# Optimization experiments

Measured on AMD Instinct MI355X. Metric: run time of the kernel, lower is better.

## Reference

```python
import jax, jax.numpy as jnp
from jax import lax
import numpy as np

TAU_R = 1.0
TAU_W = 5.0
W_MIN, W_MAX = 0.0, 0.05
N_MBON, N_FBN, N_DAN, N_KC = 20, 60, 20, 200
N_RECUR = N_MBON + N_FBN + N_DAN
B, T = 256, 61


def setup_inputs() -> dict:
    key = jax.random.key(0)
    ks = jax.random.split(key, 8)
    r_kc = jax.random.uniform(ks[0], (B, N_KC, T), dtype=jnp.float32)
    r_ext = jax.random.uniform(ks[1], (B, 2, T), dtype=jnp.float32)
    time = jnp.arange(T, dtype=jnp.float32) * 0.5  # dt = 0.5
    # KC->MBON plastic weights start at the max value (0.05), as in init
    W0_W = jax.random.uniform(ks[2], (B, N_MBON, N_KC), dtype=jnp.float32) * W_MAX
    W0_w = jax.random.uniform(ks[3], (B, N_MBON, N_KC), dtype=jnp.float32) * W_MAX
    sqrt2 = np.sqrt(2.0)
    W_mbon = jax.random.normal(ks[4], (N_RECUR, N_MBON)) * np.sqrt(1.0 / (sqrt2 * N_MBON))
    W_fbn = jax.random.normal(ks[5], (N_RECUR, N_FBN)) * np.sqrt(1.0 / (sqrt2 * N_FBN))
    W_dan = jax.random.normal(ks[6], (N_RECUR, N_DAN)) * np.sqrt(1.0 / (sqrt2 * N_DAN))
    W_recur = jnp.concatenate([W_mbon, W_fbn, W_dan], axis=1).astype(jnp.float32)
    W_ext = jax.random.normal(ks[7], (N_FBN, 2), dtype=jnp.float32)
    bias = jnp.full((N_RECUR,), 0.1, dtype=jnp.float32)
    W_readout = jax.random.normal(jax.random.fold_in(key, 99), (1, N_MBON), dtype=jnp.float32) / np.sqrt(N_MBON)
    return {"r_kc": r_kc, "r_ext": r_ext, "time": time, "n_batch": B,
            "W0_W": W0_W, "W0_w": W0_w, "W_recur": W_recur, "W_ext": W_ext,
            "bias": bias, "W_readout": W_readout}


def reference(r_kc, r_ext, time, n_batch, W0_W, W0_w, W_recur, W_ext, bias, W_readout):
    n_mbon, n_kc = W0_W.shape[1], W0_W.shape[2]
    n_fbn = W_ext.shape[0]
    n_recur = W_recur.shape[0]
    n_dan = n_recur - n_mbon - n_fbn
    nb = r_kc.shape[0]
    dt = time[1] - time[0]

    # initial state: FBN/DAN at 0.1, MBON at 0
    r_init = jnp.full((nb, n_recur), 0.1, dtype=r_kc.dtype).at[:, :n_mbon].set(0.0)
    # DAN->MBON weights are zeroed
    Wr = W_recur.at[:n_mbon, -n_dan:].set(0.0)
    rbk0 = r_kc[:, :, 0]            # KC eligibility trace
    rbd0 = r_init[:, -n_dan:]       # DAN eligibility trace
    readout0 = jnp.einsum('om,bm->bo', W_readout, r_init[:, :n_mbon]).squeeze(-1)
    zeros_dan = jnp.zeros((nb, n_dan), dtype=r_kc.dtype)

    def step(carry, xs):
        r, W, wt, rbk, rbd = carry
        rk_t, re_t = xs                                   # [B,n_kc], [B,n_ext]
        I_kc = jnp.einsum('bmk,bk->bm', W, rk_t)          # KC -> MBON via plastic W
        I_fbn = jnp.einsum('fe,be->bf', W_ext, re_t)      # context -> FBN
        I_tot = jnp.concatenate([I_kc, I_fbn, zeros_dan], axis=1)
        Wr_prod = jnp.einsum('sr,br->bs', Wr, r)
        dr = (-r + jax.nn.relu(Wr_prod + bias + I_tot)) / TAU_R
        r_new = r + dr * dt
        # plasticity update (uses the *new* DAN activity)
        rbk_new = rbk + (rk_t - rbk) * dt / TAU_W
        r_dan = r_new[:, -n_dan:]
        rbd_new = rbd + (r_dan - rbd) * dt / TAU_W
        dw = (jnp.einsum('bd,bk->bdk', rbd_new, rk_t)
              - jnp.einsum('bd,bk->bdk', r_dan, rbk_new))
        wt_new = wt + dw * dt
        W_new = jnp.clip(W + (-W + wt_new) / TAU_W * dt, W_MIN, W_MAX)
        ro = jnp.einsum('om,bm->bo', W_readout, r_new[:, :n_mbon]).squeeze(-1)
        return (r_new, W_new, wt_new, rbk_new, rbd_new), (r_new, W_new, wt_new, ro)

    xs = (jnp.moveaxis(r_kc, 2, 0)[:-1], jnp.moveaxis(r_ext, 2, 0)[:-1])
    carry0 = (r_init, W0_W, W0_w, rbk0, rbd0)
    _, (r_s, W_s, wt_s, ro_s) = lax.scan(step, carry0, xs)
    r_series = jnp.concatenate([r_init[None], r_s], axis=0)    # [T,B,n_recur]
    W_series = jnp.concatenate([W0_W[None], W_s], axis=0)      # [T,B,n_mbon,n_kc]
    wt_series = jnp.concatenate([W0_w[None], wt_s], axis=0)    # [T,B,n_mbon,n_kc]
    readout = jnp.concatenate([readout0[None], ro_s], axis=0)  # [T,B]
    return r_series, W_series, wt_series, readout
```

## Files before the change

kernel.cpp:

```cpp
#include <hip/hip_runtime.h>


#define NKC   200
#define NREC  100
#define TSTEP 61
#define NSTEP 60
#define PSTR  52
#define NTHR  512

typedef float vfloat4 __attribute__((ext_vector_type(4)));

__device__ __forceinline__ void bar_lds() {
    __builtin_amdgcn_sched_barrier(0);
    asm volatile("s_waitcnt lgkmcnt(0)");
    __builtin_amdgcn_s_barrier();
    __builtin_amdgcn_sched_barrier(0);
}

__device__ __forceinline__ void nt_store4(float* p, float4 v) {
    vfloat4 t;
    t.x = v.x; t.y = v.y; t.z = v.z; t.w = v.w;
    __builtin_nontemporal_store(t, (vfloat4*)p);
}
__device__ __forceinline__ void nt_store1(float* p, float v) {
    __builtin_nontemporal_store(v, p);
}

__global__ __launch_bounds__(NTHR, 1) void cond_rnn_kernel(
    const float* __restrict__ r_kc, const float* __restrict__ r_ext,
    const float* __restrict__ timev, const float* __restrict__ W0_W,
    const float* __restrict__ W0_w, const float* __restrict__ W_recur,
    const float* __restrict__ W_ext, const float* __restrict__ bias,
    const float* __restrict__ W_readout, float* __restrict__ out, int B)
{
    int b = blockIdx.x;
    if ((B & 7) == 0) {
        const int cpx = B >> 3;
        b = (blockIdx.x & 7) * cpx + (blockIdx.x >> 3);
    }
    const int tid = threadIdx.x;
    const float dt  = timev[1] - timev[0];
    const float dtw = dt / 5.0f;

    __shared__ __align__(16) float s_rk[TSTEP * NKC];
    __shared__ __align__(16) float s_re[128];
    __shared__ __align__(16) float s_Wro[32];
    __shared__ __align__(16) float s_r[2][112];
    __shared__ __align__(16) float s_rbd[32];
    __shared__ __align__(16) float s_part[20 * PSTR];

    const float* rk_b = r_kc + (size_t)b * (NKC * TSTEP);
    for (int f = tid; f < NKC * TSTEP; f += NTHR) {
        int k = f / TSTEP, t = f - k * TSTEP;
        s_rk[t * NKC + k] = rk_b[f];
    }
    const float* re_b = r_ext + (size_t)b * (2 * TSTEP);
    if (tid < 2 * TSTEP) s_re[tid] = re_b[tid];

    float4 wrreg[25];
    if (tid < 100) {
        const float* wrow = W_recur + tid * NREC;
        #pragma unroll
        for (int j4 = 0; j4 < 25; ++j4)
            wrreg[j4] = *(const float4*)(wrow + 4 * j4);
        if (tid < 20) {
            #pragma unroll
            for (int j4 = 20; j4 < 25; ++j4) {
                wrreg[j4].x = 0.f; wrreg[j4].y = 0.f;
                wrreg[j4].z = 0.f; wrreg[j4].w = 0.f;
            }
        }
    }

    if (tid < 20)  s_Wro[tid] = W_readout[tid];
    if (tid < 100) s_r[0][tid] = (tid < 20) ? 0.f : 0.1f;
    if (tid < 20)  s_rbd[tid] = 0.1f;

    float my_bias = 0.f, we0 = 0.f, we1 = 0.f;
    if (tid < 100) my_bias = bias[tid];
    if (tid >= 20 && tid < 80) { we0 = W_ext[(tid - 20) * 2]; we1 = W_ext[(tid - 20) * 2 + 1]; }
    float rbd_mine = 0.1f;
    float r_mine   = (tid < 20) ? 0.f : 0.1f;

    float* out_r  = out;
    float* out_W  = out + (size_t)TSTEP * B * 100;
    float* out_wt = out_W + (size_t)TSTEP * B * 4000;
    float* out_ro = out_wt + (size_t)TSTEP * B * 4000;

    float4 Wreg[2], wtreg[2], rbkreg[2], rkc[2];
    const float* W0Wb = W0_W + (size_t)b * 4000;
    const float* W0wb = W0_w + (size_t)b * 4000;
    #pragma unroll
    for (int i = 0; i < 2; ++i) {
        int c = tid + NTHR * i;
        if (c < 1000) {
            Wreg[i]  = *(const float4*)(W0Wb + 4 * c);
            wtreg[i] = *(const float4*)(W0wb + 4 * c);
            nt_store4(out_W  + (size_t)b * 4000 + 4 * c, Wreg[i]);
            nt_store4(out_wt + (size_t)b * 4000 + 4 * c, wtreg[i]);
        }
    }
    if (tid < 100) nt_store1(out_r + (size_t)b * 100 + tid, r_mine);

    __syncthreads();

    #pragma unroll
    for (int i = 0; i < 2; ++i) {
        int c = tid + NTHR * i;
        if (c < 1000) {
            int k0 = (4 * c) % NKC;
            int m  = c / 50;
            float4 rk0 = *(const float4*)(s_rk + k0);
            rbkreg[i] = rk0;
            rkc[i]    = rk0;
            float4 w = Wreg[i];
            s_part[m * PSTR + (c % 50)] =
                w.x * rk0.x + w.y * rk0.y + w.z * rk0.z + w.w * rk0.w;
        }
    }
    if (tid == 255) {
        float ro = 0.f;
        #pragma unroll
        for (int mm = 0; mm < 20; ++mm) ro += s_Wro[mm] * s_r[0][mm];
        nt_store1(out_ro + b, ro);
    }
    __syncthreads();

    for (int it = 0; it < NSTEP; ++it) {
        const int cur = it & 1, nxt = cur ^ 1;

        if (tid < 100) {
            float acc = my_bias;
            if (tid < 20) {
                const float* pp = s_part + tid * PSTR;
                float4 s01 = *(const float4*)(pp + 0)  + *(const float4*)(pp + 4);
                float4 s23 = *(const float4*)(pp + 8)  + *(const float4*)(pp + 12);
                float4 s45 = *(const float4*)(pp + 16) + *(const float4*)(pp + 20);
                float4 s67 = *(const float4*)(pp + 24) + *(const float4*)(pp + 28);
                float4 s89 = *(const float4*)(pp + 32) + *(const float4*)(pp + 36);
                float4 sab = *(const float4*)(pp + 40) + *(const float4*)(pp + 44);
                float4 t0 = s01 + s23;
                float4 t1 = s45 + s67;
                float4 t2 = s89 + sab;
                float4 u  = t0 + t1;
                u = u + t2;
                float tail = (pp[48] + pp[49]);
                acc += ((u.x + u.y) + (u.z + u.w)) + tail;
            } else if (tid < 80) {
                acc = fmaf(we0, s_re[it], acc);
                acc = fmaf(we1, s_re[TSTEP + it], acc);
            }
            float a0 = 0.f, a1 = 0.f, a2 = 0.f, a3 = 0.f;
            #pragma unroll
            for (int j4 = 0; j4 < 24; j4 += 4) {
                {
                    float4 w4 = wrreg[j4];
                    float4 r4 = *(const float4*)(&s_r[cur][4 * j4]);
                    a0 = fmaf(w4.x, r4.x, a0); a0 = fmaf(w4.y, r4.y, a0);
                    a0 = fmaf(w4.z, r4.z, a0); a0 = fmaf(w4.w, r4.w, a0);
                }
                {
                    float4 w4 = wrreg[j4 + 1];
                    float4 r4 = *(const float4*)(&s_r[cur][4 * (j4 + 1)]);
                    a1 = fmaf(w4.x, r4.x, a1); a1 = fmaf(w4.y, r4.y, a1);
                    a1 = fmaf(w4.z, r4.z, a1); a1 = fmaf(w4.w, r4.w, a1);
                }
                {
                    float4 w4 = wrreg[j4 + 2];
                    float4 r4 = *(const float4*)(&s_r[cur][4 * (j4 + 2)]);
                    a2 = fmaf(w4.x, r4.x, a2); a2 = fmaf(w4.y, r4.y, a2);
                    a2 = fmaf(w4.z, r4.z, a2); a2 = fmaf(w4.w, r4.w, a2);
                }
                {
                    float4 w4 = wrreg[j4 + 3];
                    float4 r4 = *(const float4*)(&s_r[cur][4 * (j4 + 3)]);
                    a3 = fmaf(w4.x, r4.x, a3); a3 = fmaf(w4.y, r4.y, a3);
                    a3 = fmaf(w4.z, r4.z, a3); a3 = fmaf(w4.w, r4.w, a3);
                }
            }
            {
                float4 w4 = wrreg[24];
                float4 r4 = *(const float4*)(&s_r[cur][96]);
                a0 = fmaf(w4.x, r4.x, a0); a0 = fmaf(w4.y, r4.y, a0);
                a0 = fmaf(w4.z, r4.z, a0); a0 = fmaf(w4.w, r4.w, a0);
            }
            acc += (a0 + a1) + (a2 + a3);
            float drive = acc > 0.f ? acc : 0.f;
            float rn = r_mine + dt * (drive - r_mine);
            r_mine = rn;
            s_r[nxt][tid] = rn;
            nt_store1(out_r + (size_t)(it + 1) * B * 100 + (size_t)b * 100 + tid, rn);
            if (tid >= 80) {
                rbd_mine += (rn - rbd_mine) * dtw;
                s_rbd[tid - 80] = rbd_mine;
            }
        }
        bar_lds();

        float* oW  = out_W  + (size_t)(it + 1) * B * 4000 + (size_t)b * 4000;
        float* owt = out_wt + (size_t)(it + 1) * B * 4000 + (size_t)b * 4000;
        const float* rk_nx  = s_rk + (it + 1) * NKC;
        #pragma unroll
        for (int i = 0; i < 2; ++i) {
            int c = tid + NTHR * i;
            if (c < 1000) {
                int k0 = (4 * c) % NKC;
                int m  = c / 50;
                float4 rk4 = rkc[i];
                float4 rkn = *(const float4*)(rk_nx + k0);
                rkc[i] = rkn;
                float rbdn = s_rbd[m];
                float rdan = s_r[nxt][80 + m];
                float4 rb = rbkreg[i];
                rb.x += (rk4.x - rb.x) * dtw;  rb.y += (rk4.y - rb.y) * dtw;
                rb.z += (rk4.z - rb.z) * dtw;  rb.w += (rk4.w - rb.w) * dtw;
                rbkreg[i] = rb;
                float4 wt = wtreg[i];
                wt.x = fmaf(rbdn * rk4.x - rdan * rb.x, dt, wt.x);
                wt.y = fmaf(rbdn * rk4.y - rdan * rb.y, dt, wt.y);
                wt.z = fmaf(rbdn * rk4.z - rdan * rb.z, dt, wt.z);
                wt.w = fmaf(rbdn * rk4.w - rdan * rb.w, dt, wt.w);
                wtreg[i] = wt;
                float4 w = Wreg[i];
                w.x += (wt.x - w.x) * dtw;  w.y += (wt.y - w.y) * dtw;
                w.z += (wt.z - w.z) * dtw;  w.w += (wt.w - w.w) * dtw;
                w.x = fminf(fmaxf(w.x, 0.f), 0.05f);
                w.y = fminf(fmaxf(w.y, 0.f), 0.05f);
                w.z = fminf(fmaxf(w.z, 0.f), 0.05f);
                w.w = fminf(fmaxf(w.w, 0.f), 0.05f);
                Wreg[i] = w;
                s_part[m * PSTR + (c % 50)] =
                    w.x * rkn.x + w.y * rkn.y + w.z * rkn.z + w.w * rkn.w;
                nt_store4(owt + 4 * c, wt);
                nt_store4(oW  + 4 * c, w);
            }
        }
        if (tid == 255) {
            const float* rr = &s_r[nxt][0];
            float q0 = 0.f, q1 = 0.f, q2 = 0.f, q3 = 0.f;
            #pragma unroll
            for (int mm = 0; mm < 20; mm += 4) {
                q0 = fmaf(s_Wro[mm],     rr[mm],     q0);
                q1 = fmaf(s_Wro[mm + 1], rr[mm + 1], q1);
                q2 = fmaf(s_Wro[mm + 2], rr[mm + 2], q2);
                q3 = fmaf(s_Wro[mm + 3], rr[mm + 3], q3);
            }
            nt_store1(out_ro + (size_t)(it + 1) * B + b, (q0 + q1) + (q2 + q3));
        }
        bar_lds();
    }
}

extern "C" void kernel_launch(void* const* d_in, const int* in_sizes, int n_in,
                              void* d_out, int out_size, void* d_ws, size_t ws_size,
                              hipStream_t stream) {
    const float* r_kc      = (const float*)d_in[0];
    const float* r_ext     = (const float*)d_in[1];
    const float* timev     = (const float*)d_in[2];
    const float* W0_W      = (const float*)d_in[4];
    const float* W0_w      = (const float*)d_in[5];
    const float* W_recur   = (const float*)d_in[6];
    const float* W_ext     = (const float*)d_in[7];
    const float* bias      = (const float*)d_in[8];
    const float* W_readout = (const float*)d_in[9];

    const int B = in_sizes[0] / (NKC * TSTEP);
    cond_rnn_kernel<<<dim3(B), dim3(NTHR), 0, stream>>>(
        r_kc, r_ext, timev, W0_W, W0_w, W_recur, W_ext, bias, W_readout,
        (float*)d_out, B);
}
```

Measured before the change: 510.6 us.

## Recompute DAN rates redundantly per wave to drop one barrier per step

Every wave now computes the 20 DAN neuron updates and eligibility traces itself, reading DAN recurrent weight rows from LDS, and broadcasts them with lane shuffles. This removes the mid-step barrier that separated the recurrent update from the plasticity update. The partial-sum buffer is double-buffered so the next step's MBON reduction does not race with current writes, and the readout is computed by wave 0 via shuffles. In exchange, every wave does extra redundant dot-product work and uses more LDS.

New measurement: 1.410 ms. 2.76x slower.

```diff
diff --git a/kernel.cpp b/kernel.cpp
--- a/kernel.cpp
+++ b/kernel.cpp
@@ -38,7 +38,8 @@
         const int cpx = B >> 3;
         b = (blockIdx.x & 7) * cpx + (blockIdx.x >> 3);
     }
-    const int tid = threadIdx.x;
+    const int tid  = threadIdx.x;
+    const int lane = tid & 63;
     const float dt  = timev[1] - timev[0];
     const float dtw = dt / 5.0f;
 
@@ -46,8 +47,8 @@
     __shared__ __align__(16) float s_re[128];
     __shared__ __align__(16) float s_Wro[32];
     __shared__ __align__(16) float s_r[2][112];
-    __shared__ __align__(16) float s_rbd[32];
-    __shared__ __align__(16) float s_part[20 * PSTR];
+    __shared__ __align__(16) float s_Wrd[20 * 100];
+    __shared__ __align__(16) float s_part2[2][20 * PSTR];
 
     const float* rk_b = r_kc + (size_t)b * (NKC * TSTEP);
     for (int f = tid; f < NKC * TSTEP; f += NTHR) {
@@ -56,6 +57,8 @@
     }
     const float* re_b = r_ext + (size_t)b * (2 * TSTEP);
     if (tid < 2 * TSTEP) s_re[tid] = re_b[tid];
+    for (int f = tid; f < 20 * 100; f += NTHR)
+        s_Wrd[f] = W_recur[80 * NREC + f];
 
     float4 wrreg[25];
     if (tid < 100) {
@@ -74,13 +77,15 @@
 
     if (tid < 20)  s_Wro[tid] = W_readout[tid];
     if (tid < 100) s_r[0][tid] = (tid < 20) ? 0.f : 0.1f;
-    if (tid < 20)  s_rbd[tid] = 0.1f;
 
     float my_bias = 0.f, we0 = 0.f, we1 = 0.f;
     if (tid < 100) my_bias = bias[tid];
     if (tid >= 20 && tid < 80) { we0 = W_ext[(tid - 20) * 2]; we1 = W_ext[(tid - 20) * 2 + 1]; }
-    float rbd_mine = 0.1f;
-    float r_mine   = (tid < 20) ? 0.f : 0.1f;
+    float r_mine = (tid < 20) ? 0.f : 0.1f;
+
+    const int  drow     = (lane < 20) ? lane : 0;
+    const float dan_bias = bias[80 + drow];
+    float dan_rbd = 0.1f;
 
     float* out_r  = out;
     float* out_W  = out + (size_t)TSTEP * B * 100;
@@ -114,7 +119,7 @@
             rbkreg[i] = rk0;
             rkc[i]    = rk0;
             float4 w = Wreg[i];
-            s_part[m * PSTR + (c % 50)] =
+            s_part2[0][m * PSTR + (c % 50)] =
                 w.x * rk0.x + w.y * rk0.y + w.z * rk0.z + w.w * rk0.w;
         }
     }
@@ -129,10 +134,56 @@
     for (int it = 0; it < NSTEP; ++it) {
         const int cur = it & 1, nxt = cur ^ 1;
 
+        float dan_rn;
+        {
+            float a0 = 0.f, a1 = 0.f, a2 = 0.f, a3 = 0.f;
+            const float* wd = s_Wrd + drow * 100;
+            #pragma unroll
+            for (int j4 = 0; j4 < 24; j4 += 4) {
+                {
+                    float4 w4 = *(const float4*)(wd + 4 * j4);
+                    float4 r4 = *(const float4*)(&s_r[cur][4 * j4]);
+                    a0 = fmaf(w4.x, r4.x, a0); a0 = fmaf(w4.y, r4.y, a0);
+                    a0 = fmaf(w4.z, r4.z, a0); a0 = fmaf(w4.w, r4.w, a0);
+                }
+                {
+                    float4 w4 = *(const float4*)(wd + 4 * (j4 + 1));
+                    float4 r4 = *(const float4*)(&s_r[cur][4 * (j4 + 1)]);
+                    a1 = fmaf(w4.x, r4.x, a1); a1 = fmaf(w4.y, r4.y, a1);
+                    a1 = fmaf(w4.z, r4.z, a1); a1 = fmaf(w4.w, r4.w, a1);
+                }
+                {
+                    float4 w4 = *(const float4*)(wd + 4 * (j4 + 2));
+                    float4 r4 = *(const float4*)(&s_r[cur][4 * (j4 + 2)]);
+                    a2 = fmaf(w4.x, r4.x, a2); a2 = fmaf(w4.y, r4.y, a2);
+                    a2 = fmaf(w4.z, r4.z, a2); a2 = fmaf(w4.w, r4.w, a2);
+                }
+                {
+                    float4 w4 = *(const float4*)(wd + 4 * (j4 + 3));
+                    float4 r4 = *(const float4*)(&s_r[cur][4 * (j4 + 3)]);
+                    a3 = fmaf(w4.x, r4.x, a3); a3 = fmaf(w4.y, r4.y, a3);
+                    a3 = fmaf(w4.z, r4.z, a3); a3 = fmaf(w4.w, r4.w, a3);
+                }
+            }
+            {
+                float4 w4 = *(const float4*)(wd + 96);
+                float4 r4 = *(const float4*)(&s_r[cur][96]);
+                a0 = fmaf(w4.x, r4.x, a0); a0 = fmaf(w4.y, r4.y, a0);
+                a0 = fmaf(w4.z, r4.z, a0); a0 = fmaf(w4.w, r4.w, a0);
+            }
+            float acc = dan_bias;
+            acc += (a0 + a1) + (a2 + a3);
+            float drive = acc > 0.f ? acc : 0.f;
+            float rdp = s_r[cur][80 + drow];
+            dan_rn = rdp + dt * (drive - rdp);
+            dan_rbd += (dan_rn - dan_rbd) * dtw;
+        }
+
+        float rnA = 0.f;
         if (tid < 100) {
             float acc = my_bias;
             if (tid < 20) {
-                const float* pp = s_part + tid * PSTR;
+                const float* pp = s_part2[cur] + tid * PSTR;
                 float4 s01 = *(const float4*)(pp + 0)  + *(const float4*)(pp + 4);
                 float4 s23 = *(const float4*)(pp + 8)  + *(const float4*)(pp + 12);
                 float4 s45 = *(const float4*)(pp + 16) + *(const float4*)(pp + 20);
@@ -188,29 +239,25 @@
             float drive = acc > 0.f ? acc : 0.f;
             float rn = r_mine + dt * (drive - r_mine);
             r_mine = rn;
+            rnA = rn;
             s_r[nxt][tid] = rn;
             nt_store1(out_r + (size_t)(it + 1) * B * 100 + (size_t)b * 100 + tid, rn);
-            if (tid >= 80) {
-                rbd_mine += (rn - rbd_mine) * dtw;
-                s_rbd[tid - 80] = rbd_mine;
-            }
-        }
-        bar_lds();
+        }
 
         float* oW  = out_W  + (size_t)(it + 1) * B * 4000 + (size_t)b * 4000;
         float* owt = out_wt + (size_t)(it + 1) * B * 4000 + (size_t)b * 4000;
-        const float* rk_nx  = s_rk + (it + 1) * NKC;
+        const float* rk_nx = s_rk + (it + 1) * NKC;
         #pragma unroll
         for (int i = 0; i < 2; ++i) {
             int c = tid + NTHR * i;
             if (c < 1000) {
                 int k0 = (4 * c) % NKC;
                 int m  = c / 50;
+                float rdan = __shfl(dan_rn,  m);
+                float rbdn = __shfl(dan_rbd, m);
                 float4 rk4 = rkc[i];
                 float4 rkn = *(const float4*)(rk_nx + k0);
                 rkc[i] = rkn;
-                float rbdn = s_rbd[m];
-                float rdan = s_r[nxt][80 + m];
                 float4 rb = rbkreg[i];
                 rb.x += (rk4.x - rb.x) * dtw;  rb.y += (rk4.y - rb.y) * dtw;
                 rb.z += (rk4.z - rb.z) * dtw;  rb.w += (rk4.w - rb.w) * dtw;
@@ -229,24 +276,26 @@
                 w.z = fminf(fmaxf(w.z, 0.f), 0.05f);
                 w.w = fminf(fmaxf(w.w, 0.f), 0.05f);
                 Wreg[i] = w;
-                s_part[m * PSTR + (c % 50)] =
+                s_part2[nxt][m * PSTR + (c % 50)] =
                     w.x * rkn.x + w.y * rkn.y + w.z * rkn.z + w.w * rkn.w;
                 nt_store4(owt + 4 * c, wt);
                 nt_store4(oW  + 4 * c, w);
             }
         }
-        if (tid == 255) {
-            const float* rr = &s_r[nxt][0];
+
+        if (tid < 64) {
             float q0 = 0.f, q1 = 0.f, q2 = 0.f, q3 = 0.f;
             #pragma unroll
             for (int mm = 0; mm < 20; mm += 4) {
-                q0 = fmaf(s_Wro[mm],     rr[mm],     q0);
-                q1 = fmaf(s_Wro[mm + 1], rr[mm + 1], q1);
-                q2 = fmaf(s_Wro[mm + 2], rr[mm + 2], q2);
-                q3 = fmaf(s_Wro[mm + 3], rr[mm + 3], q3);
-            }
-            nt_store1(out_ro + (size_t)(it + 1) * B + b, (q0 + q1) + (q2 + q3));
-        }
+                q0 = fmaf(s_Wro[mm],     __shfl(rnA, mm),     q0);
+                q1 = fmaf(s_Wro[mm + 1], __shfl(rnA, mm + 1), q1);
+                q2 = fmaf(s_Wro[mm + 2], __shfl(rnA, mm + 2), q2);
+                q3 = fmaf(s_Wro[mm + 3], __shfl(rnA, mm + 3), q3);
+            }
+            if (tid == 0)
+                nt_store1(out_ro + (size_t)(it + 1) * B + b, (q0 + q1) + (q2 + q3));
+        }
+
         bar_lds();
     }
 }
```
